# Kernel optimization log

Hardware: AMD Instinct MI355X
Metric: run time of the kernel (lower is better)

The kernel has to match this reference:

```python
import jax, jax.numpy as jnp
import numpy as np

N_NODES = 50000


def setup_inputs() -> dict:
    key = jax.random.key(0)
    k1, k2, k3, k4, k5 = jax.random.split(key, 5)
    d_in, d_out, n_edges = 128, 128, 800000
    x = jax.random.normal(k1, (N_NODES, d_in), dtype=jnp.float32)
    edge_index = jax.random.randint(k2, (2, n_edges), 0, N_NODES, dtype=jnp.int64)
    # Glorot-ish init for linear weights, bias zeros-like small normal
    W_l = jax.random.normal(k3, (d_in, d_out), dtype=jnp.float32) / np.sqrt(d_in)
    W_r = jax.random.normal(k4, (d_in, d_out), dtype=jnp.float32) / np.sqrt(d_in)
    b = jax.random.normal(k5, (d_out,), dtype=jnp.float32) * 0.01
    return {"x": x, "edge_index": edge_index, "W_l": W_l, "W_r": W_r, "b": b}


def reference(x, edge_index, W_l, W_r, b):
    # PyG SAGEConv (aggr='mean', root_weight=True, bias=True):
    #   out_i = W_l @ mean_{j: (j->i) in E} x_j + b + W_r @ x_i
    # followed by ReLU (GConv act) and dropout(p=0.0, eval) == identity.
    src, dst = edge_index[0], edge_index[1]
    msgs = x[src]                                            # [E, d_in] gather
    agg_sum = jax.ops.segment_sum(msgs, dst, num_segments=N_NODES)  # [N, d_in]
    deg = jax.ops.segment_sum(jnp.ones_like(dst, dtype=x.dtype), dst,
                              num_segments=N_NODES)          # [N]
    agg_mean = agg_sum / jnp.maximum(deg, 1.0)[:, None]      # zero for isolated nodes
    z = agg_mean @ W_l + b + x @ W_r                         # [N, d_out]
    return jax.nn.relu(z)
```

## Files before the change

kernel.cpp:

```cpp
#include <hip/hip_runtime.h>

#define N_NODES 50000
#define D 128
#define NC 256
#define SCANB 196
#define AGG_NB 782
#define CONV_NB 1563

typedef short bf16x8 __attribute__((ext_vector_type(8)));
typedef float f32x4 __attribute__((ext_vector_type(4)));
typedef float f32x2 __attribute__((ext_vector_type(2)));
typedef unsigned char uchar;

__device__ __forceinline__ ushort f2bf(float f) {
    uint u = __float_as_uint(f);
    u += 0x7FFF + ((u >> 16) & 1);
    return (ushort)(u >> 16);
}

__device__ __forceinline__ void addrow_fp8(int4 q, float* a) {
    f32x2 p;
    p = __builtin_amdgcn_cvt_pk_f32_fp8(q.x, false); a[0]  += p.x; a[1]  += p.y;
    p = __builtin_amdgcn_cvt_pk_f32_fp8(q.x, true);  a[2]  += p.x; a[3]  += p.y;
    p = __builtin_amdgcn_cvt_pk_f32_fp8(q.y, false); a[4]  += p.x; a[5]  += p.y;
    p = __builtin_amdgcn_cvt_pk_f32_fp8(q.y, true);  a[6]  += p.x; a[7]  += p.y;
    p = __builtin_amdgcn_cvt_pk_f32_fp8(q.z, false); a[8]  += p.x; a[9]  += p.y;
    p = __builtin_amdgcn_cvt_pk_f32_fp8(q.z, true);  a[10] += p.x; a[11] += p.y;
    p = __builtin_amdgcn_cvt_pk_f32_fp8(q.w, false); a[12] += p.x; a[13] += p.y;
    p = __builtin_amdgcn_cvt_pk_f32_fp8(q.w, true);  a[14] += p.x; a[15] += p.y;
}

__global__ __launch_bounds__(1024) void fused_count_convert(
        const float* __restrict__ x, const float* __restrict__ Wl,
        const float* __restrict__ Wr, const int* __restrict__ dst,
        ushort* __restrict__ x_bf, int* __restrict__ x_fp8,
        ushort* __restrict__ Btf, uchar* __restrict__ cum,
        int E, int chunk) {
    const int b = blockIdx.x;
    const int t = threadIdx.x;
    if (b < NC) {
        __shared__ uint cnt[N_NODES / 4];
        for (int k = t; k < N_NODES / 4; k += 1024) cnt[k] = 0;
        __syncthreads();
        const int e0 = b * chunk;
        const int e1 = min(E, e0 + chunk);
        for (int e = e0 + t; e < e1; e += 1024) {
            int d = dst[e];
            atomicAdd(&cnt[d >> 2], 1u << ((d & 3) << 3));
        }
        __syncthreads();
        uint* pu = (uint*)(cum + (size_t)b * N_NODES);
        for (int k = t; k < N_NODES / 4; k += 1024) pu[k] = cnt[k];
    } else {
        const int i = (b - NC) * 1024 + t;
        if (i < (N_NODES * D) / 4) {
            float4 v = ((const float4*)x)[i];
            ushort4 o;
            o.x = f2bf(v.x); o.y = f2bf(v.y); o.z = f2bf(v.z); o.w = f2bf(v.w);
            ((ushort4*)x_bf)[i] = o;
            int p = __builtin_amdgcn_cvt_pk_fp8_f32(v.x, v.y, 0, false);
            p = __builtin_amdgcn_cvt_pk_fp8_f32(v.z, v.w, p, true);
            const int node = i >> 5;
            const int fq = i & 31;
            const int h = fq >> 4;
            x_fp8[h * N_NODES * 16 + node * 16 + (fq & 15)] = p;
        }
        if (i < 32768) {
            int j  = i & 7;
            int l  = (i >> 3) & 63;
            int nf = (i >> 9) & 7;
            int ks = (i >> 12) & 7;
            int lr = l & 15, kb = l >> 4;
            int col  = nf * 16 + lr;
            int kloc = (ks & 3) * 32 + kb * 8 + j;
            const float* W = (ks < 4) ? Wl : Wr;
            Btf[i] = f2bf(W[kloc * D + col]);
        }
    }
}

__global__ __launch_bounds__(256) void scanAB_kernel(uchar* __restrict__ cum,
                                                     int* __restrict__ offsets,
                                                     int* __restrict__ blocksums) {
    __shared__ int wsums[4];
    __shared__ int wbase[4];
    const int t = threadIdx.x;
    const int lane = t & 63;
    const int wid = t >> 6;
    const int n = blockIdx.x * 256 + t;

    int s = 0;
    if (n < N_NODES) {
        #pragma unroll 4
        for (int c = 0; c < NC; ++c) {
            int v = (int)cum[(size_t)c * N_NODES + n];
            cum[(size_t)c * N_NODES + n] = (uchar)s;
            s += v;
        }
    }
    int sc = s;
    #pragma unroll
    for (int off = 1; off < 64; off <<= 1) {
        int u = __shfl_up(sc, off);
        if (lane >= off) sc += u;
    }
    if (lane == 63) wsums[wid] = sc;
    __syncthreads();
    if (t == 0) {
        int c = 0;
        #pragma unroll
        for (int w = 0; w < 4; ++w) { int tmp = wsums[w]; wbase[w] = c; c += tmp; }
        blocksums[blockIdx.x] = c;
    }
    __syncthreads();
    if (n < N_NODES) offsets[n] = wbase[wid] + sc - s;
}

__global__ __launch_bounds__(256) void scanBC2_kernel(int* __restrict__ offsets,
                                                      const int* __restrict__ blocksums,
                                                      int E) {
    __shared__ int ws2[4];
    __shared__ int sbase;
    const int t = threadIdx.x;
    const int lane = t & 63;
    const int wid = t >> 6;
    const int b = blockIdx.x;
    int v = (t < b) ? blocksums[t] : 0;
    #pragma unroll
    for (int off = 32; off > 0; off >>= 1) v += __shfl_down(v, off);
    if (lane == 0) ws2[wid] = v;
    __syncthreads();
    if (t == 0) sbase = ws2[0] + ws2[1] + ws2[2] + ws2[3];
    __syncthreads();
    const int n = b * 256 + t;
    if (n < N_NODES) offsets[n] += sbase;
    if (b == SCANB - 1 && t == 0) offsets[N_NODES] = E;
}

__global__ __launch_bounds__(1024) void scatterC_kernel(const int* __restrict__ src,
                                                        const int* __restrict__ dst,
                                                        const int* __restrict__ offsets,
                                                        const uchar* __restrict__ cum,
                                                        ushort* __restrict__ sorted_src,
                                                        int E, int chunk) {
    __shared__ uint cnt[N_NODES / 4];
    const int t = threadIdx.x;
    const int b = blockIdx.x;
    for (int k = t; k < N_NODES / 4; k += 1024) cnt[k] = 0;
    __syncthreads();
    const uchar* cb = cum + (size_t)b * N_NODES;
    const int e0 = b * chunk;
    const int e1 = min(E, e0 + chunk);
    for (int e = e0 + t; e < e1; e += 1024) {
        int d = dst[e];
        uint prev = atomicAdd(&cnt[d >> 2], 1u << ((d & 3) << 3));
        int lrank = (int)((prev >> ((d & 3) << 3)) & 0xFFu);
        int pos = offsets[d] + (int)cb[d] + lrank;
        sorted_src[pos] = (ushort)src[e];
    }
}

__global__ __launch_bounds__(256) void aggregate_fp8(const int* __restrict__ x_fp8,
                                                     const ushort* __restrict__ sorted_src,
                                                     const int* __restrict__ offsets,
                                                     ushort* __restrict__ agg_bf) {
    const int b = blockIdx.x;
    const int half = (b >= AGG_NB) ? 1 : 0;
    const int nb = b - half * AGG_NB;
    const int t = threadIdx.x;
    const int g = t >> 2;
    const int j = t & 3;
    const int node = nb * 64 + g;
    if (node >= N_NODES) return;
    const int s = offsets[node];
    const int e = offsets[node + 1];

    const int4* xq = (const int4*)(x_fp8 + half * N_NODES * 16);

    float a[16];
    #pragma unroll
    for (int k = 0; k < 16; ++k) a[k] = 0.0f;

    int p = s;
    for (; p + 4 <= e; p += 4) {
        int s0 = sorted_src[p + 0];
        int s1 = sorted_src[p + 1];
        int s2 = sorted_src[p + 2];
        int s3 = sorted_src[p + 3];
        int4 q0 = xq[s0 * 4 + j];
        int4 q1 = xq[s1 * 4 + j];
        int4 q2 = xq[s2 * 4 + j];
        int4 q3 = xq[s3 * 4 + j];
        addrow_fp8(q0, a); addrow_fp8(q1, a); addrow_fp8(q2, a); addrow_fp8(q3, a);
    }
    for (; p < e; ++p) {
        int s0 = sorted_src[p];
        int4 q0 = xq[s0 * 4 + j];
        addrow_fp8(q0, a);
    }

    const int dcnt = e - s;
    const float scale = (dcnt > 0) ? (1.0f / (float)dcnt) : 0.0f;
    ushort tmp[16];
    #pragma unroll
    for (int k = 0; k < 16; ++k) tmp[k] = f2bf(a[k] * scale);
    *(int4*)&agg_bf[node * D + half * 64 + j * 16]     = ((int4*)tmp)[0];
    *(int4*)&agg_bf[node * D + half * 64 + j * 16 + 8] = ((int4*)tmp)[1];
}

__global__ __launch_bounds__(256) void gemm_direct(const ushort* __restrict__ agg_bf,
                                                   const ushort* __restrict__ x_bf,
                                                   const ushort* __restrict__ Btf,
                                                   const float* __restrict__ bias,
                                                   float* __restrict__ out) {
    const int t = threadIdx.x;
    const int w = t >> 6;
    const int l = t & 63;
    const int lr = l & 15;
    const int kb = l >> 4;
    const int n0 = blockIdx.x * 64;

    int r = n0 + w * 16 + lr;
    if (r >= N_NODES) r = N_NODES - 1;

    f32x4 acc[8] = {};

    #pragma unroll
    for (int ks = 0; ks < 8; ++ks) {
        bf16x8 af = (ks < 4)
            ? *(const bf16x8*)&agg_bf[r * D + ks * 32 + kb * 8]
            : *(const bf16x8*)&x_bf[r * D + (ks - 4) * 32 + kb * 8];
        const ushort* bp = Btf + (size_t)(ks * 8 * 64 + l) * 8;
        #pragma unroll
        for (int nf = 0; nf < 8; ++nf) {
            bf16x8 bfr = *(const bf16x8*)&bp[nf * 64 * 8];
            acc[nf] = __builtin_amdgcn_mfma_f32_16x16x32_bf16(af, bfr, acc[nf], 0, 0, 0);
        }
    }

    #pragma unroll
    for (int nf = 0; nf < 8; ++nf) {
        const int col = nf * 16 + lr;
        const float bb = bias[col];
        #pragma unroll
        for (int i = 0; i < 4; ++i) {
            int row = n0 + w * 16 + kb * 4 + i;
            if (row < N_NODES)
                out[row * D + col] = fmaxf(acc[nf][i] + bb, 0.0f);
        }
    }
}

extern "C" void kernel_launch(void* const* d_in, const int* in_sizes, int n_in,
                              void* d_out, int out_size, void* d_ws, size_t ws_size,
                              hipStream_t stream) {
    const float* x  = (const float*)d_in[0];
    const int*   ei = (const int*)d_in[1];
    const float* Wl = (const float*)d_in[2];
    const float* Wr = (const float*)d_in[3];
    const float* b  = (const float*)d_in[4];
    float* out = (float*)d_out;

    const int E = in_sizes[1] / 2;
    const int* src = ei;
    const int* dst = ei + E;
    const int chunk = (E + NC - 1) / NC;

    char* wsp = (char*)d_ws;
    int*    offsets   = (int*)(wsp + 0);
    int*    blocksums = (int*)(wsp + 200704);
    ushort* sorted    = (ushort*)(wsp + 201728);
    uchar*  cum       = (uchar*)(wsp + 1801760);
    ushort* x_bf      = (ushort*)(wsp + 14601760);
    int*    x_fp8     = (int*)(wsp + 27401760);
    ushort* agg_bf    = (ushort*)(wsp + 33801760);
    ushort* Btf       = (ushort*)(wsp + 46601760);

    fused_count_convert<<<NC + CONV_NB, 1024, 0, stream>>>(
        x, Wl, Wr, dst, x_bf, x_fp8, Btf, cum, E, chunk);
    scanAB_kernel<<<SCANB, 256, 0, stream>>>(cum, offsets, blocksums);
    scanBC2_kernel<<<SCANB, 256, 0, stream>>>(offsets, blocksums, E);
    scatterC_kernel<<<NC, 1024, 0, stream>>>(src, dst, offsets, cum, sorted, E, chunk);
    aggregate_fp8<<<2 * AGG_NB, 256, 0, stream>>>(x_fp8, sorted, offsets, agg_bf);
    gemm_direct<<<(N_NODES + 63) / 64, 256, 0, stream>>>(agg_bf, x_bf, Btf, b, out);
}
```

Before: 103.9 us.

## Fold block-sum scan into scatter and aggregate kernels, drop scanBC2 launch

```diff
diff --git a/kernel.cpp b/kernel.cpp
--- a/kernel.cpp
+++ b/kernel.cpp
@@ -116,37 +116,24 @@
     if (n < N_NODES) offsets[n] = wbase[wid] + sc - s;
 }
 
-__global__ __launch_bounds__(256) void scanBC2_kernel(int* __restrict__ offsets,
-                                                      const int* __restrict__ blocksums,
-                                                      int E) {
-    __shared__ int ws2[4];
-    __shared__ int sbase;
-    const int t = threadIdx.x;
-    const int lane = t & 63;
-    const int wid = t >> 6;
-    const int b = blockIdx.x;
-    int v = (t < b) ? blocksums[t] : 0;
-    #pragma unroll
-    for (int off = 32; off > 0; off >>= 1) v += __shfl_down(v, off);
-    if (lane == 0) ws2[wid] = v;
-    __syncthreads();
-    if (t == 0) sbase = ws2[0] + ws2[1] + ws2[2] + ws2[3];
-    __syncthreads();
-    const int n = b * 256 + t;
-    if (n < N_NODES) offsets[n] += sbase;
-    if (b == SCANB - 1 && t == 0) offsets[N_NODES] = E;
-}
-
 __global__ __launch_bounds__(1024) void scatterC_kernel(const int* __restrict__ src,
                                                         const int* __restrict__ dst,
                                                         const int* __restrict__ offsets,
+                                                        const int* __restrict__ blocksums,
                                                         const uchar* __restrict__ cum,
                                                         ushort* __restrict__ sorted_src,
                                                         int E, int chunk) {
     __shared__ uint cnt[N_NODES / 4];
+    __shared__ int base[SCANB];
     const int t = threadIdx.x;
     const int b = blockIdx.x;
     for (int k = t; k < N_NODES / 4; k += 1024) cnt[k] = 0;
+    if (t < SCANB) base[t] = blocksums[t];
+    __syncthreads();
+    if (t == 0) {
+        int run = 0;
+        for (int k = 0; k < SCANB; ++k) { int v = base[k]; base[k] = run; run += v; }
+    }
     __syncthreads();
     const uchar* cb = cum + (size_t)b * N_NODES;
     const int e0 = b * chunk;
@@ -155,7 +142,7 @@
         int d = dst[e];
         uint prev = atomicAdd(&cnt[d >> 2], 1u << ((d & 3) << 3));
         int lrank = (int)((prev >> ((d & 3) << 3)) & 0xFFu);
-        int pos = offsets[d] + (int)cb[d] + lrank;
+        int pos = offsets[d] + base[d >> 8] + (int)cb[d] + lrank;
         sorted_src[pos] = (ushort)src[e];
     }
 }
@@ -163,17 +150,32 @@
 __global__ __launch_bounds__(256) void aggregate_fp8(const int* __restrict__ x_fp8,
                                                      const ushort* __restrict__ sorted_src,
                                                      const int* __restrict__ offsets,
-                                                     ushort* __restrict__ agg_bf) {
+                                                     const int* __restrict__ blocksums,
+                                                     ushort* __restrict__ agg_bf, int E) {
+    __shared__ int base[SCANB];
     const int b = blockIdx.x;
-    const int half = (b >= AGG_NB) ? 1 : 0;
-    const int nb = b - half * AGG_NB;
-    const int t = threadIdx.x;
+    const int r = b & 7;
+    const int q = b >> 3;
+    const int half = (r >= 4) ? 1 : 0;
+    const int nb = q * 4 + (r & 3);
+    const int t = threadIdx.x;
+
+    if (t < SCANB) base[t] = blocksums[t];
+    __syncthreads();
+    if (t == 0) {
+        int run = 0;
+        for (int k = 0; k < SCANB; ++k) { int v = base[k]; base[k] = run; run += v; }
+    }
+    __syncthreads();
+    if (nb >= AGG_NB) return;
+
     const int g = t >> 2;
     const int j = t & 3;
     const int node = nb * 64 + g;
     if (node >= N_NODES) return;
-    const int s = offsets[node];
-    const int e = offsets[node + 1];
+    const int s = offsets[node] + base[node >> 8];
+    const int np = node + 1;
+    const int e = (np < N_NODES) ? (offsets[np] + base[np >> 8]) : E;
 
     const int4* xq = (const int4*)(x_fp8 + half * N_NODES * 16);
 
@@ -279,8 +281,9 @@
     fused_count_convert<<<NC + CONV_NB, 1024, 0, stream>>>(
         x, Wl, Wr, dst, x_bf, x_fp8, Btf, cum, E, chunk);
     scanAB_kernel<<<SCANB, 256, 0, stream>>>(cum, offsets, blocksums);
-    scanBC2_kernel<<<SCANB, 256, 0, stream>>>(offsets, blocksums, E);
-    scatterC_kernel<<<NC, 1024, 0, stream>>>(src, dst, offsets, cum, sorted, E, chunk);
-    aggregate_fp8<<<2 * AGG_NB, 256, 0, stream>>>(x_fp8, sorted, offsets, agg_bf);
+    scatterC_kernel<<<NC, 1024, 0, stream>>>(src, dst, offsets, blocksums, cum,
+                                             sorted, E, chunk);
+    aggregate_fp8<<<8 * SCANB, 256, 0, stream>>>(x_fp8, sorted, offsets, blocksums,
+                                                 agg_bf, E);
     gemm_direct<<<(N_NODES + 63) / 64, 256, 0, stream>>>(agg_bf, x_bf, Btf, b, out);
 }
```

Measured after the change: 102.9 us. Within noise of the previous version (-0.9%).
